# Performance work log

Hardware: AMD Instinct MI355X
Metric: run time of the kernel (lower is better)

The kernel has to match this reference:

```python
import jax, jax.numpy as jnp
import numpy as np

MARGIN = 0.2
EPS = 1e-6  # torch.pairwise_distance default eps added to (x1 - x2)


def setup_inputs() -> dict:
    key = jax.random.key(0)
    k1, k2 = jax.random.split(key)
    N, D = 8192, 128
    x = jax.random.normal(k1, (N, D), dtype=jnp.float32)
    target = jax.random.randint(k2, (N,), 0, 1000)
    return {"x": x, "target": target}


def _pairwise_dist(x):
    # torch.pairwise_distance(x.unsqueeze(0), x.unsqueeze(1)):
    #   diff[i, j] = x[j] - x[i] + EPS ; dist[i, j] = ||diff[i, j]||_2
    # Expanded quadratic form avoids the [N, N, D] diff tensor:
    #   ||a - b + e||^2 = ||a||^2 + ||b||^2 - 2 a.b + 2e*sum(a - b) + D*e^2
    sq = jnp.sum(x * x, axis=1)          # [N]
    s = jnp.sum(x, axis=1)               # [N]
    dot = x @ x.T                        # [N, N]
    D = x.shape[1]
    d2 = (sq[None, :] + sq[:, None] - 2.0 * dot
          + 2.0 * EPS * (s[None, :] - s[:, None]) + D * EPS * EPS)
    return jnp.sqrt(jnp.maximum(d2, 0.0))


def reference(x, target):
    N = x.shape[0]
    dist = _pairwise_dist(x)                                 # [N, N]
    same = target[None, :] == target[:, None]                # [N, N] bool
    pos_mask = (same & ~jnp.eye(N, dtype=bool)).astype(x.dtype)
    hardest_pos = jnp.max(pos_mask * dist, axis=1, keepdims=True)  # [N, 1]
    neg_mask = (~same).astype(x.dtype)
    max_neg = jnp.max(dist, axis=1, keepdims=True)           # [N, 1]
    anchor_neg = dist + max_neg * (1.0 - neg_mask)           # push positives up
    hardest_neg = jnp.min(anchor_neg, axis=1, keepdims=True) # [N, 1]
    loss = jax.nn.relu(hardest_pos - hardest_neg + MARGIN)
    return jnp.mean(loss)
```

## Files before the change

### kernel.cpp

```cpp
#include <hip/hip_runtime.h>

#define N 8192
#define Dk 128
#define NC 1024
#define EPSC 1e-6f
#define MARGIN 0.2f

typedef __attribute__((ext_vector_type(8))) short bf16x8;
typedef __attribute__((ext_vector_type(4))) float f32x4;

__device__ __forceinline__ unsigned short f2bf(float f) {
    unsigned u = __float_as_uint(f);
    u = (u + 0x7FFFu + ((u >> 16) & 1u)) >> 16;
    return (unsigned short)u;
}

__global__ void hist_kernel(const int* __restrict__ tgt, int* __restrict__ hist) {
    int i = blockIdx.x * 256 + threadIdx.x;
    atomicAdd(&hist[tgt[i]], 1);
}

__global__ void scan_kernel(const int* __restrict__ hist, int* __restrict__ pref,
                            int* __restrict__ cursor) {
    __shared__ int tmp[NC];
    int t = threadIdx.x;
    int h = hist[t];
    tmp[t] = h;
    __syncthreads();
#pragma unroll
    for (int off = 1; off < NC; off <<= 1) {
        int v = (t >= off) ? tmp[t - off] : 0;
        __syncthreads();
        tmp[t] += v;
        __syncthreads();
    }
    int ex = tmp[t] - h;
    pref[t] = ex;
    cursor[t] = ex;
}

__global__ void scatter_kernel(const int* __restrict__ tgt, const int* __restrict__ pref,
                               const int* __restrict__ hist, int* __restrict__ cursor,
                               int* __restrict__ perm, uint2* __restrict__ band,
                               int* __restrict__ cls) {
    int i = blockIdx.x * 256 + threadIdx.x;
    int c = tgt[i];
    int pos = atomicAdd(&cursor[c], 1);
    perm[pos] = i;
    uint2 b;
    b.x = (unsigned)pref[c];
    b.y = (unsigned)(pref[c] + hist[c]);
    band[pos] = b;
    cls[pos] = c;
}

__global__ void prep_kernel(const float* __restrict__ x, const int* __restrict__ perm,
                            const int* __restrict__ cls,
                            uint4* __restrict__ Frag, uint2* __restrict__ QT,
                            float* __restrict__ P) {
    int wv = blockIdx.x * 4 + (threadIdx.x >> 6);
    int lane = threadIdx.x & 63;
    int k = wv * 4 + (lane >> 4);
    int c = lane & 15;
    int orig = perm[k];
    const float4* x4 = reinterpret_cast<const float4*>(x);
    float4 v0 = x4[orig * 32 + c * 2];
    float4 v1 = x4[orig * 32 + c * 2 + 1];
    float sq = v0.x * v0.x + v0.y * v0.y + v0.z * v0.z + v0.w * v0.w +
               v1.x * v1.x + v1.y * v1.y + v1.z * v1.z + v1.w * v1.w;
    float s = v0.x + v0.y + v0.z + v0.w + v1.x + v1.y + v1.z + v1.w;
    ushort4 lo, hi;
    lo.x = f2bf(v0.x); lo.y = f2bf(v0.y); lo.z = f2bf(v0.z); lo.w = f2bf(v0.w);
    hi.x = f2bf(v1.x); hi.y = f2bf(v1.y); hi.z = f2bf(v1.z); hi.w = f2bf(v1.w);
    uint4 pk;
    pk.x = (unsigned)lo.x | ((unsigned)lo.y << 16);
    pk.y = (unsigned)lo.z | ((unsigned)lo.w << 16);
    pk.z = (unsigned)hi.x | ((unsigned)hi.y << 16);
    pk.w = (unsigned)hi.z | ((unsigned)hi.w << 16);
    Frag[((k >> 4) * 4 + (c >> 2)) * 64 + (c & 3) * 16 + (k & 15)] = pk;
#pragma unroll
    for (int m = 1; m <= 8; m <<= 1) {
        sq += __shfl_xor(sq, m);
        s += __shfl_xor(s, m);
    }
    if (c == 0) {
        P[k] = sq - 2.0f * EPSC * s;
        float Qj = sq + 2.0f * EPSC * s + (float)Dk * EPSC * EPSC;
        uint2 qt;
        qt.x = __float_as_uint(-0.5f * Qj);
        qt.y = (unsigned)cls[k];
        QT[k] = qt;
    }
}

#define LOADB(Bb, qq, t)                       \
    do {                                       \
        const int jt_ = jt0 + (t);             \
        Bb[0] = Fr[(jt_ * 4 + 0) * 64 + lane]; \
        Bb[1] = Fr[(jt_ * 4 + 1) * 64 + lane]; \
        Bb[2] = Fr[(jt_ * 4 + 2) * 64 + lane]; \
        Bb[3] = Fr[(jt_ * 4 + 3) * 64 + lane]; \
        qq = QT[jt_ * 16 + n];                 \
    } while (0)

#define COMPUTE(Bb, qq, t)                                                            \
    do {                                                                              \
        const float Qv_ = __uint_as_float(qq.x);                        \
        f32x4 acc[4];                                                                 \
        acc[0] = Qv_; acc[1] = Qv_; acc[2] = Qv_; acc[3] = Qv_;                       \
        _Pragma("unroll")                                                             \
        for (int kk = 0; kk < 4; ++kk) {                                              \
            _Pragma("unroll")                                                         \
            for (int ti = 0; ti < 4; ++ti)                                            \
                acc[ti] = __builtin_amdgcn_mfma_f32_16x16x32_bf16(Af[ti][kk], Bb[kk], \
                                                                  acc[ti], 0, 0, 0);  \
        }                                                                             \
        const int jc_ = (jt0 + (t)) * 16;                                             \
        if (jc_ < bHi && jc_ + 16 > bLo) {      \
            const int tv_ = (int)qq.y;                                                \
            _Pragma("unroll")                                                         \
            for (int ti = 0; ti < 4; ++ti) {                                          \
                f32x4 v = acc[ti];                                                    \
                int e0 = tv_ == tsl[4 * ti + 0];                                      \
                int e1 = tv_ == tsl[4 * ti + 1];                                      \
                int e2 = tv_ == tsl[4 * ti + 2];                                      \
                int e3 = tv_ == tsl[4 * ti + 3];                                      \
                hp[4 * ti + 0] = fminf(hp[4 * ti + 0], e0 ? v[0] : INFINITY);         \
                hp[4 * ti + 1] = fminf(hp[4 * ti + 1], e1 ? v[1] : INFINITY);         \
                hp[4 * ti + 2] = fminf(hp[4 * ti + 2], e2 ? v[2] : INFINITY);         \
                hp[4 * ti + 3] = fminf(hp[4 * ti + 3], e3 ? v[3] : INFINITY);         \
                mn[4 * ti + 0] = fmaxf(mn[4 * ti + 0], e0 ? -INFINITY : v[0]);        \
                mn[4 * ti + 1] = fmaxf(mn[4 * ti + 1], e1 ? -INFINITY : v[1]);        \
                mn[4 * ti + 2] = fmaxf(mn[4 * ti + 2], e2 ? -INFINITY : v[2]);        \
                mn[4 * ti + 3] = fmaxf(mn[4 * ti + 3], e3 ? -INFINITY : v[3]);        \
            }                                                                         \
        } else {                  \
            _Pragma("unroll")                                                         \
            for (int ti = 0; ti < 4; ++ti) {                                          \
                mn[4 * ti + 0] = fmaxf(mn[4 * ti + 0], acc[ti][0]);                   \
                mn[4 * ti + 1] = fmaxf(mn[4 * ti + 1], acc[ti][1]);                   \
                mn[4 * ti + 2] = fmaxf(mn[4 * ti + 2], acc[ti][2]);                   \
                mn[4 * ti + 3] = fmaxf(mn[4 * ti + 3], acc[ti][3]);                   \
            }                                                                         \
        }                                                                             \
    } while (0)

__global__ __launch_bounds__(256, 2) void main_kernel(
        const uint4* __restrict__ Frag, const uint2* __restrict__ QT,
        const int* __restrict__ cls, const uint2* __restrict__ band,
        float* __restrict__ partHp, float* __restrict__ partMn) {
    const int w = threadIdx.x >> 6;
    const int lane = threadIdx.x & 63;
    const int n = lane & 15;
    const int q = lane >> 4;

    const int ig = (int)blockIdx.x >> 3;
    const int jg = (int)blockIdx.x & 7;
    const int rbase = ig * 64;
    const int jt0 = jg * 64 + w * 16;

    const bf16x8* Fr = reinterpret_cast<const bf16x8*>(Frag);

    const int bLo = (int)band[rbase].x;
    const int bHi = (int)band[rbase + 63].y;

    bf16x8 Af[4][4];
#pragma unroll
    for (int ti = 0; ti < 4; ++ti)
#pragma unroll
        for (int kk = 0; kk < 4; ++kk)
            Af[ti][kk] = Fr[((ig * 4 + ti) * 4 + kk) * 64 + lane];

    int tsl[16];
#pragma unroll
    for (int ti = 0; ti < 4; ++ti) {
        int4 t4 = *reinterpret_cast<const int4*>(&cls[rbase + 16 * ti + 4 * q]);
        tsl[4 * ti + 0] = t4.x;
        tsl[4 * ti + 1] = t4.y;
        tsl[4 * ti + 2] = t4.z;
        tsl[4 * ti + 3] = t4.w;
    }

    float hp[16], mn[16];
#pragma unroll
    for (int s = 0; s < 16; ++s) {
        hp[s] = INFINITY;
        mn[s] = -INFINITY;
    }

    bf16x8 B0[4], B1[4], B2[4];
    uint2 q0, q1, q2;
    LOADB(B0, q0, 0);
    LOADB(B1, q1, 1);
    LOADB(B2, q2, 2);
#pragma unroll
    for (int tt = 0; tt < 15; tt += 3) {
        COMPUTE(B0, q0, tt);
        if (tt + 3 < 16) LOADB(B0, q0, tt + 3);
        COMPUTE(B1, q1, tt + 1);
        if (tt + 4 < 16) LOADB(B1, q1, tt + 4);
        COMPUTE(B2, q2, tt + 2);
        if (tt + 5 < 16) LOADB(B2, q2, tt + 5);
    }
    COMPUTE(B0, q0, 15);

#pragma unroll
    for (int m = 1; m <= 8; m <<= 1) {
#pragma unroll
        for (int s = 0; s < 16; ++s) {
            hp[s] = fminf(hp[s], __shfl_xor(hp[s], m));
            mn[s] = fmaxf(mn[s], __shfl_xor(mn[s], m));
        }
    }
    if (n == 0) {
        const int wg = jg * 4 + w;
#pragma unroll
        for (int ti = 0; ti < 4; ++ti)
#pragma unroll
            for (int r = 0; r < 4; ++r) {
                int i = rbase + 16 * ti + 4 * q + r;
                partHp[wg * N + i] = hp[4 * ti + r];
                partMn[wg * N + i] = mn[4 * ti + r];
            }
    }
}

__global__ void finish_kernel(const float* __restrict__ P,
                              const float* __restrict__ partHp,
                              const float* __restrict__ partMn,
                              float* __restrict__ out) {
    int i = blockIdx.x * 256 + threadIdx.x;
    float hpm = INFINITY, mnm = -INFINITY;
#pragma unroll
    for (int wg = 0; wg < 32; ++wg) {
        hpm = fminf(hpm, partHp[wg * N + i]);
        mnm = fmaxf(mnm, partMn[wg * N + i]);
    }
    float Pi = P[i];
    float hp = sqrtf(fmaxf(fmaf(-2.0f, hpm, Pi), 0.0f));
    float hn = sqrtf(fmaxf(fmaf(-2.0f, mnm, Pi), 0.0f));
    float sum = fmaxf(hp - hn + MARGIN, 0.0f) * (1.0f / (float)N);
#pragma unroll
    for (int m = 32; m >= 1; m >>= 1) sum += __shfl_xor(sum, m);
    __shared__ float ws[4];
    int lane = threadIdx.x & 63, wv = threadIdx.x >> 6;
    if (lane == 0) ws[wv] = sum;
    __syncthreads();
    if (threadIdx.x == 0) atomicAdd(out, ws[0] + ws[1] + ws[2] + ws[3]);
}

extern "C" void kernel_launch(void* const* d_in, const int* in_sizes, int n_in,
                              void* d_out, int out_size, void* d_ws, size_t ws_size,
                              hipStream_t stream) {
    const float* x = (const float*)d_in[0];
    const int* tgt = (const int*)d_in[1];
    float* out = (float*)d_out;

    char* ws = (char*)d_ws;
    size_t off = 0;
    uint4* Frag = (uint4*)(ws + off); off += (size_t)N * Dk * 2;
    uint2* QT = (uint2*)(ws + off); off += (size_t)N * 8;
    float* P = (float*)(ws + off); off += (size_t)N * 4;
    float* partHp = (float*)(ws + off); off += (size_t)32 * N * 4;
    float* partMn = (float*)(ws + off); off += (size_t)32 * N * 4;
    uint2* band = (uint2*)(ws + off); off += (size_t)N * 8;
    int* perm = (int*)(ws + off); off += (size_t)N * 4;
    int* cls = (int*)(ws + off); off += (size_t)N * 4;
    int* hist = (int*)(ws + off); off += NC * 4;
    int* pref = (int*)(ws + off); off += NC * 4;
    int* cursor = (int*)(ws + off); off += NC * 4;

    hipMemsetAsync(hist, 0, NC * 4, stream);
    hipMemsetAsync(d_out, 0, sizeof(float), stream);
    hist_kernel<<<N / 256, 256, 0, stream>>>(tgt, hist);
    scan_kernel<<<1, NC, 0, stream>>>(hist, pref, cursor);
    scatter_kernel<<<N / 256, 256, 0, stream>>>(tgt, pref, hist, cursor, perm, band, cls);
    prep_kernel<<<N / 16, 256, 0, stream>>>(x, perm, cls, Frag, QT, P);
    main_kernel<<<1024, 256, 0, stream>>>(Frag, QT, cls, band, partHp, partMn);
    finish_kernel<<<32, 256, 0, stream>>>(P, partHp, partMn, out);
}
```

Baseline: 105.3 us.

## Transpose MFMA operands, share column tiles across waves, double-buffer accumulators

Swaps the MFMA operand order so each lane's accumulator holds four column values for a single row. This lets the min/max reduction happen in-register, with a cheaper cross-lane reduce and fewer partial writes. Each block now covers 256 rows with four waves sharing the same 16 column tiles, and the Q bias becomes a per-column f32x4 vector load. The epilogue of tile t-1 is software-pipelined against the MFMAs of tile t using two accumulator sets, at the cost of extra register pressure.

Result: faster. 102.7 us (-2.4%).

```diff
diff --git a/kernel.cpp b/kernel.cpp
--- a/kernel.cpp
+++ b/kernel.cpp
@@ -55,8 +55,7 @@
 }
 
 __global__ void prep_kernel(const float* __restrict__ x, const int* __restrict__ perm,
-                            const int* __restrict__ cls,
-                            uint4* __restrict__ Frag, uint2* __restrict__ QT,
+                            uint4* __restrict__ Frag, float* __restrict__ Qh,
                             float* __restrict__ P) {
     int wv = blockIdx.x * 4 + (threadIdx.x >> 6);
     int lane = threadIdx.x & 63;
@@ -85,68 +84,67 @@
     }
     if (c == 0) {
         P[k] = sq - 2.0f * EPSC * s;
-        float Qj = sq + 2.0f * EPSC * s + (float)Dk * EPSC * EPSC;
-        uint2 qt;
-        qt.x = __float_as_uint(-0.5f * Qj);
-        qt.y = (unsigned)cls[k];
-        QT[k] = qt;
-    }
-}
-
-#define LOADB(Bb, qq, t)                       \
-    do {                                       \
-        const int jt_ = jt0 + (t);             \
-        Bb[0] = Fr[(jt_ * 4 + 0) * 64 + lane]; \
-        Bb[1] = Fr[(jt_ * 4 + 1) * 64 + lane]; \
-        Bb[2] = Fr[(jt_ * 4 + 2) * 64 + lane]; \
-        Bb[3] = Fr[(jt_ * 4 + 3) * 64 + lane]; \
-        qq = QT[jt_ * 16 + n];                 \
-    } while (0)
-
-#define COMPUTE(Bb, qq, t)                                                            \
+        Qh[k] = -0.5f * (sq + 2.0f * EPSC * s + (float)Dk * EPSC * EPSC);
+    }
+}
+
+#define LOADB(Bb, Qq, t)                                                \
+    do {                                                                \
+        const int jt_ = jt0 + (t);                                      \
+        Bb[0] = Fr[(jt_ * 4 + 0) * 64 + lane];                          \
+        Bb[1] = Fr[(jt_ * 4 + 1) * 64 + lane];                          \
+        Bb[2] = Fr[(jt_ * 4 + 2) * 64 + lane];                          \
+        Bb[3] = Fr[(jt_ * 4 + 3) * 64 + lane];                          \
+        Qq = *reinterpret_cast<const f32x4*>(&Qh[jt_ * 16 + 4 * q]);    \
+    } while (0)
+
+#define MFMA16(ACC, Bb, Qq)                                                           \
     do {                                                                              \
-        const float Qv_ = __uint_as_float(qq.x);                        \
-        f32x4 acc[4];                                                                 \
-        acc[0] = Qv_; acc[1] = Qv_; acc[2] = Qv_; acc[3] = Qv_;                       \
         _Pragma("unroll")                                                             \
-        for (int kk = 0; kk < 4; ++kk) {                                              \
-            _Pragma("unroll")                                                         \
-            for (int ti = 0; ti < 4; ++ti)                                            \
-                acc[ti] = __builtin_amdgcn_mfma_f32_16x16x32_bf16(Af[ti][kk], Bb[kk], \
-                                                                  acc[ti], 0, 0, 0);  \
+        for (int ti = 0; ti < 4; ++ti) {                                              \
+            ACC[ti] = __builtin_amdgcn_mfma_f32_16x16x32_bf16(Bb[0], Af[ti][0], Qq, 0, 0, 0); \
+            ACC[ti] = __builtin_amdgcn_mfma_f32_16x16x32_bf16(Bb[1], Af[ti][1], ACC[ti], 0, 0, 0); \
+            ACC[ti] = __builtin_amdgcn_mfma_f32_16x16x32_bf16(Bb[2], Af[ti][2], ACC[ti], 0, 0, 0); \
+            ACC[ti] = __builtin_amdgcn_mfma_f32_16x16x32_bf16(Bb[3], Af[ti][3], ACC[ti], 0, 0, 0); \
         }                                                                             \
+    } while (0)
+
+#define EPILOGUE(ACC, t)                                                              \
+    do {                                                                              \
         const int jc_ = (jt0 + (t)) * 16;                                             \
-        if (jc_ < bHi && jc_ + 16 > bLo) {      \
-            const int tv_ = (int)qq.y;                                                \
+        if (jc_ < bHi && jc_ + 16 > bLo) {     \
+            int4 cj = *reinterpret_cast<const int4*>(&cls[jc_ + 4 * q]);              \
             _Pragma("unroll")                                                         \
             for (int ti = 0; ti < 4; ++ti) {                                          \
-                f32x4 v = acc[ti];                                                    \
-                int e0 = tv_ == tsl[4 * ti + 0];                                      \
-                int e1 = tv_ == tsl[4 * ti + 1];                                      \
-                int e2 = tv_ == tsl[4 * ti + 2];                                      \
-                int e3 = tv_ == tsl[4 * ti + 3];                                      \
-                hp[4 * ti + 0] = fminf(hp[4 * ti + 0], e0 ? v[0] : INFINITY);         \
-                hp[4 * ti + 1] = fminf(hp[4 * ti + 1], e1 ? v[1] : INFINITY);         \
-                hp[4 * ti + 2] = fminf(hp[4 * ti + 2], e2 ? v[2] : INFINITY);         \
-                hp[4 * ti + 3] = fminf(hp[4 * ti + 3], e3 ? v[3] : INFINITY);         \
-                mn[4 * ti + 0] = fmaxf(mn[4 * ti + 0], e0 ? -INFINITY : v[0]);        \
-                mn[4 * ti + 1] = fmaxf(mn[4 * ti + 1], e1 ? -INFINITY : v[1]);        \
-                mn[4 * ti + 2] = fmaxf(mn[4 * ti + 2], e2 ? -INFINITY : v[2]);        \
-                mn[4 * ti + 3] = fmaxf(mn[4 * ti + 3], e3 ? -INFINITY : v[3]);        \
+                f32x4 v = ACC[ti];                                                    \
+                int mc = myc[ti];                                                     \
+                hp[ti] = fminf(hp[ti], cj.x == mc ? v[0] : INFINITY);                 \
+                hp[ti] = fminf(hp[ti], cj.y == mc ? v[1] : INFINITY);                 \
+                hp[ti] = fminf(hp[ti], cj.z == mc ? v[2] : INFINITY);                 \
+                hp[ti] = fminf(hp[ti], cj.w == mc ? v[3] : INFINITY);                 \
+                mn[ti] = fmaxf(mn[ti], cj.x == mc ? -INFINITY : v[0]);                \
+                mn[ti] = fmaxf(mn[ti], cj.y == mc ? -INFINITY : v[1]);                \
+                mn[ti] = fmaxf(mn[ti], cj.z == mc ? -INFINITY : v[2]);                \
+                mn[ti] = fmaxf(mn[ti], cj.w == mc ? -INFINITY : v[3]);                \
             }                                                                         \
-        } else {                  \
+        } else {                \
             _Pragma("unroll")                                                         \
             for (int ti = 0; ti < 4; ++ti) {                                          \
-                mn[4 * ti + 0] = fmaxf(mn[4 * ti + 0], acc[ti][0]);                   \
-                mn[4 * ti + 1] = fmaxf(mn[4 * ti + 1], acc[ti][1]);                   \
-                mn[4 * ti + 2] = fmaxf(mn[4 * ti + 2], acc[ti][2]);                   \
-                mn[4 * ti + 3] = fmaxf(mn[4 * ti + 3], acc[ti][3]);                   \
+                f32x4 v = ACC[ti];                                                    \
+                mn[ti] = fmaxf(mn[ti], fmaxf(fmaxf(v[0], v[1]), fmaxf(v[2], v[3])));  \
             }                                                                         \
         }                                                                             \
     } while (0)
 
+#define STEP(t, ACCc, ACCp, Bc, Qc, Bp, Qp)   \
+    do {                                      \
+        MFMA16(ACCc, Bc, Qc);                 \
+        if ((t) + 2 < 16) LOADB(Bp, Qp, (t) + 2); \
+        if ((t) > 0) EPILOGUE(ACCp, (t) - 1); \
+    } while (0)
+
 __global__ __launch_bounds__(256, 2) void main_kernel(
-        const uint4* __restrict__ Frag, const uint2* __restrict__ QT,
+        const uint4* __restrict__ Frag, const float* __restrict__ Qh,
         const int* __restrict__ cls, const uint2* __restrict__ band,
         float* __restrict__ partHp, float* __restrict__ partMn) {
     const int w = threadIdx.x >> 6;
@@ -154,74 +152,73 @@
     const int n = lane & 15;
     const int q = lane >> 4;
 
-    const int ig = (int)blockIdx.x >> 3;
-    const int jg = (int)blockIdx.x & 7;
-    const int rbase = ig * 64;
-    const int jt0 = jg * 64 + w * 16;
+    const int ig = (int)blockIdx.x >> 5;
+    const int jg = (int)blockIdx.x & 31;
+    const int rw = ig * 256 + 64 * w;
+    const int jt0 = jg * 16;
 
     const bf16x8* Fr = reinterpret_cast<const bf16x8*>(Frag);
 
-    const int bLo = (int)band[rbase].x;
-    const int bHi = (int)band[rbase + 63].y;
+    const int bLo = (int)band[rw].x;
+    const int bHi = (int)band[rw + 63].y;
 
     bf16x8 Af[4][4];
 #pragma unroll
     for (int ti = 0; ti < 4; ++ti)
 #pragma unroll
         for (int kk = 0; kk < 4; ++kk)
-            Af[ti][kk] = Fr[((ig * 4 + ti) * 4 + kk) * 64 + lane];
-
-    int tsl[16];
-#pragma unroll
-    for (int ti = 0; ti < 4; ++ti) {
-        int4 t4 = *reinterpret_cast<const int4*>(&cls[rbase + 16 * ti + 4 * q]);
-        tsl[4 * ti + 0] = t4.x;
-        tsl[4 * ti + 1] = t4.y;
-        tsl[4 * ti + 2] = t4.z;
-        tsl[4 * ti + 3] = t4.w;
-    }
-
-    float hp[16], mn[16];
-#pragma unroll
-    for (int s = 0; s < 16; ++s) {
+            Af[ti][kk] = Fr[(((rw >> 4) + ti) * 4 + kk) * 64 + lane];
+
+    int myc[4];
+#pragma unroll
+    for (int ti = 0; ti < 4; ++ti) myc[ti] = cls[rw + 16 * ti + n];
+
+    float hp[4], mn[4];
+#pragma unroll
+    for (int s = 0; s < 4; ++s) {
         hp[s] = INFINITY;
         mn[s] = -INFINITY;
     }
 
     bf16x8 B0[4], B1[4], B2[4];
-    uint2 q0, q1, q2;
-    LOADB(B0, q0, 0);
-    LOADB(B1, q1, 1);
-    LOADB(B2, q2, 2);
-#pragma unroll
-    for (int tt = 0; tt < 15; tt += 3) {
-        COMPUTE(B0, q0, tt);
-        if (tt + 3 < 16) LOADB(B0, q0, tt + 3);
-        COMPUTE(B1, q1, tt + 1);
-        if (tt + 4 < 16) LOADB(B1, q1, tt + 4);
-        COMPUTE(B2, q2, tt + 2);
-        if (tt + 5 < 16) LOADB(B2, q2, tt + 5);
-    }
-    COMPUTE(B0, q0, 15);
-
-#pragma unroll
-    for (int m = 1; m <= 8; m <<= 1) {
-#pragma unroll
-        for (int s = 0; s < 16; ++s) {
+    f32x4 Q0, Q1, Q2;
+    f32x4 accA[4], accB[4];
+
+    LOADB(B0, Q0, 0);
+    LOADB(B1, Q1, 1);
+    STEP(0, accA, accB, B0, Q0, B2, Q2);
+    STEP(1, accB, accA, B1, Q1, B0, Q0);
+    STEP(2, accA, accB, B2, Q2, B1, Q1);
+    STEP(3, accB, accA, B0, Q0, B2, Q2);
+    STEP(4, accA, accB, B1, Q1, B0, Q0);
+    STEP(5, accB, accA, B2, Q2, B1, Q1);
+    STEP(6, accA, accB, B0, Q0, B2, Q2);
+    STEP(7, accB, accA, B1, Q1, B0, Q0);
+    STEP(8, accA, accB, B2, Q2, B1, Q1);
+    STEP(9, accB, accA, B0, Q0, B2, Q2);
+    STEP(10, accA, accB, B1, Q1, B0, Q0);
+    STEP(11, accB, accA, B2, Q2, B1, Q1);
+    STEP(12, accA, accB, B0, Q0, B2, Q2);
+    STEP(13, accB, accA, B1, Q1, B0, Q0);
+    STEP(14, accA, accB, B2, Q2, B1, Q1);
+    STEP(15, accB, accA, B0, Q0, B2, Q2);
+    EPILOGUE(accB, 15);
+
+#pragma unroll
+    for (int m = 16; m <= 32; m <<= 1) {
+#pragma unroll
+        for (int s = 0; s < 4; ++s) {
             hp[s] = fminf(hp[s], __shfl_xor(hp[s], m));
             mn[s] = fmaxf(mn[s], __shfl_xor(mn[s], m));
         }
     }
-    if (n == 0) {
-        const int wg = jg * 4 + w;
-#pragma unroll
-        for (int ti = 0; ti < 4; ++ti)
-#pragma unroll
-            for (int r = 0; r < 4; ++r) {
-                int i = rbase + 16 * ti + 4 * q + r;
-                partHp[wg * N + i] = hp[4 * ti + r];
-                partMn[wg * N + i] = mn[4 * ti + r];
-            }
+    if (q == 0) {
+#pragma unroll
+        for (int ti = 0; ti < 4; ++ti) {
+            int i = rw + 16 * ti + n;
+            partHp[jg * N + i] = hp[ti];
+            partMn[jg * N + i] = mn[ti];
+        }
     }
 }
 
@@ -259,7 +256,7 @@
     char* ws = (char*)d_ws;
     size_t off = 0;
     uint4* Frag = (uint4*)(ws + off); off += (size_t)N * Dk * 2;
-    uint2* QT = (uint2*)(ws + off); off += (size_t)N * 8;
+    float* Qh = (float*)(ws + off); off += (size_t)N * 4;
     float* P = (float*)(ws + off); off += (size_t)N * 4;
     float* partHp = (float*)(ws + off); off += (size_t)32 * N * 4;
     float* partMn = (float*)(ws + off); off += (size_t)32 * N * 4;
@@ -275,7 +272,7 @@
     hist_kernel<<<N / 256, 256, 0, stream>>>(tgt, hist);
     scan_kernel<<<1, NC, 0, stream>>>(hist, pref, cursor);
     scatter_kernel<<<N / 256, 256, 0, stream>>>(tgt, pref, hist, cursor, perm, band, cls);
-    prep_kernel<<<N / 16, 256, 0, stream>>>(x, perm, cls, Frag, QT, P);
-    main_kernel<<<1024, 256, 0, stream>>>(Frag, QT, cls, band, partHp, partMn);
+    prep_kernel<<<N / 16, 256, 0, stream>>>(x, perm, Frag, Qh, P);
+    main_kernel<<<1024, 256, 0, stream>>>(Frag, Qh, cls, band, partHp, partMn);
     finish_kernel<<<32, 256, 0, stream>>>(P, partHp, partMn, out);
 }
```
